# Performance work log

Hardware: AMD Instinct MI355X
Metric: run time of the kernel (lower is better)

## Reference

```python
import jax, jax.numpy as jnp
import numpy as np

B, LQ, LK = 2, 4096, 512
Q_DIM, KV_DIM, D_ATTN, N_HEADS = 1024, 1024, 1024, 16
HDIM = D_ATTN // N_HEADS
LOOKBACK = 4
ROPE_MAX = 8192


def rope_tables(smax, hdim):
    inv_freq = 1.0 / (10000.0 ** (jnp.arange(0, hdim, 2, dtype=jnp.float32) / hdim))
    freqs = jnp.arange(smax, dtype=jnp.float32)[:, None] * inv_freq[None, :]  # [S, hdim/2]
    emb = jnp.concatenate([freqs, freqs], axis=-1)  # [S, hdim]
    return jnp.cos(emb), jnp.sin(emb)


def rotate_half(x):
    h = x.shape[-1] // 2
    return jnp.concatenate([-x[..., h:], x[..., :h]], axis=-1)


def setup_inputs() -> dict:
    key = jax.random.key(0)
    ks = jax.random.split(key, 8)
    q = jax.random.normal(ks[0], (B, LQ, Q_DIM), dtype=jnp.float32)
    kv = jax.random.normal(ks[1], (B, LK, KV_DIM), dtype=jnp.float32)
    q_pos_ids = jax.random.randint(ks[2], (B, LQ), 0, 4096)
    kv_pos_ids = jax.random.randint(ks[3], (LK,), 0, 4096)
    seg_id = jnp.sort(jax.random.randint(ks[4], (B, LQ), 0, LK), axis=-1)
    sc = 1.0 / np.sqrt(Q_DIM)
    Wq = jax.random.normal(ks[5], (Q_DIM, D_ATTN), dtype=jnp.float32) * sc
    Wkv = jax.random.normal(ks[6], (KV_DIM, 2 * D_ATTN), dtype=jnp.float32) * sc
    Wo = jax.random.normal(ks[7], (D_ATTN, Q_DIM), dtype=jnp.float32) * sc
    return {"q": q, "kv": kv, "q_pos_ids": q_pos_ids, "kv_pos_ids": kv_pos_ids,
            "seg_id": seg_id, "Wq": Wq, "Wkv": Wkv, "Wo": Wo}


def reference(q, kv, q_pos_ids, kv_pos_ids, seg_id, Wq, Wkv, Wo):
    Bq, Lq, _ = q.shape
    Lk = kv.shape[1]
    # projections + split heads -> [B, H, L, hdim]
    qh = (q @ Wq).reshape(Bq, Lq, N_HEADS, HDIM).transpose(0, 2, 1, 3)
    kvl = kv @ Wkv
    kh = kvl[..., :D_ATTN].reshape(Bq, Lk, N_HEADS, HDIM).transpose(0, 2, 1, 3)
    vh = kvl[..., D_ATTN:].reshape(Bq, Lk, N_HEADS, HDIM).transpose(0, 2, 1, 3)
    # gathered RoPE
    cos, sin = rope_tables(ROPE_MAX, HDIM)  # [S, hdim]
    qp = jnp.clip(q_pos_ids, 0, ROPE_MAX - 1)
    q_cos = cos[qp][:, None]  # [B,1,Lq,hdim]
    q_sin = sin[qp][:, None]
    qh = qh * q_cos + rotate_half(qh) * q_sin
    kp = jnp.clip(kv_pos_ids, 0, ROPE_MAX - 1)
    k_cos = cos[kp][None, None]  # [1,1,Lk,hdim]
    k_sin = sin[kp][None, None]
    kh = kh * k_cos + rotate_half(kh) * k_sin
    # segment lookback mask: keep iff seg_id - lookback <= k <= seg_id
    kidx = jnp.arange(Lk)
    keep = (kidx[None, None, :] <= seg_id[:, :, None]) & \
           (kidx[None, None, :] >= seg_id[:, :, None] - LOOKBACK)  # [B,Lq,Lk]
    scale = 1.0 / np.sqrt(HDIM)
    scores = jnp.einsum('bhqd,bhkd->bhqk', qh, kh) * scale
    scores = jnp.where(keep[:, None], scores, -jnp.inf)
    attn = jax.nn.softmax(scores, axis=-1)
    ctx = jnp.einsum('bhqk,bhkd->bhqd', attn, vh)
    out = ctx.transpose(0, 2, 1, 3).reshape(Bq, Lq, D_ATTN)
    return out @ Wo
```

## Files before the change

kernel.cpp:

```cpp
#include <hip/hip_runtime.h>
#include <math.h>


typedef unsigned short u16;
typedef __attribute__((ext_vector_type(8))) short bhalf8;
typedef __attribute__((ext_vector_type(4))) float fvec4;

#define MFMA(a, b, c) __builtin_amdgcn_mfma_f32_16x16x32_bf16((a), (b), (c), 0, 0, 0)

__device__ __forceinline__ u16 f2bf(float f) {
  unsigned u = __float_as_uint(f);
  u += 0x7fffu + ((u >> 16) & 1u);
  return (u16)(u >> 16);
}
__device__ __forceinline__ float bf2f(u16 h) {
  return __uint_as_float(((unsigned)h) << 16);
}

__global__ __launch_bounds__(256) void prep_kernel(
    const float* __restrict__ Wq, const float* __restrict__ Wkv,
    const float* __restrict__ Wo, u16* __restrict__ WqT,
    u16* __restrict__ WkvT, u16* __restrict__ WoT,
    const float* __restrict__ q, u16* __restrict__ qb,
    const float* __restrict__ kv, u16* __restrict__ kvb,
    float2* __restrict__ csT) {
  const int bid = blockIdx.x;
  if (bid < 4096) {
    __shared__ float tile[32][33];
    const float* W;
    u16* Wt;
    int N, t;
    if (bid < 1024)      { W = Wq;  Wt = WqT;  N = 1024; t = bid; }
    else if (bid < 3072) { W = Wkv; Wt = WkvT; N = 2048; t = bid - 1024; }
    else                 { W = Wo;  Wt = WoT;  N = 1024; t = bid - 3072; }
    const int sh = (N >> 11) + 5;
    const int n0 = (t & ((1 << sh) - 1)) << 5;
    const int k0 = (t >> sh) << 5;
    const int tx = threadIdx.x & 31, ty = threadIdx.x >> 5;
#pragma unroll
    for (int i = 0; i < 32; i += 8)
      tile[ty + i][tx] = W[(size_t)(k0 + ty + i) * N + n0 + tx];
    __syncthreads();
#pragma unroll
    for (int i = 0; i < 32; i += 8)
      Wt[(size_t)(n0 + ty + i) * 1024 + k0 + tx] = f2bf(tile[tx][ty + i]);
    return;
  }
  const int NQ4 = 2097152, NKV4 = 262144, NR = 131072;
  const int stride = 2048 * 256;
  for (int u = (bid - 4096) * 256 + threadIdx.x; u < NQ4 + NKV4 + NR; u += stride) {
    if (u < NQ4) {
      const float4 v = ((const float4*)q)[u];
      ushort4 o;
      o.x = f2bf(v.x); o.y = f2bf(v.y); o.z = f2bf(v.z); o.w = f2bf(v.w);
      ((ushort4*)qb)[u] = o;
    } else if (u < NQ4 + NKV4) {
      const int i = u - NQ4;
      const float4 v = ((const float4*)kv)[i];
      ushort4 o;
      o.x = f2bf(v.x); o.y = f2bf(v.y); o.z = f2bf(v.z); o.w = f2bf(v.w);
      ((ushort4*)kvb)[i] = o;
    } else {
      const int i = u - NQ4 - NKV4;
      const int pos = i >> 5, j = i & 31;
      const float invf = expf(-(float)j * 0.28782313662425572f);
      float s, c;
      sincosf((float)pos * invf, &s, &c);
      csT[i] = make_float2(c, s);
    }
  }
}

__device__ __forceinline__ void gemm_core_8w(
    const u16* __restrict__ A, const u16* __restrict__ Bt,
    int m0, int n0, fvec4 acc[2][4], u16* As, u16* Bs) {
  const int tid = threadIdx.x;
  const int lane = tid & 63;
  const int wv = tid >> 6, wm = wv >> 1, wn = wv & 1;

  int a_off[2], b_off[4];
#pragma unroll
  for (int i = 0; i < 2; ++i) {
    const int rA = wm * 32 + i * 16 + (lane & 15);
    a_off[i] = rA * 32 + (((lane >> 4) ^ ((rA >> 1) & 3)) << 3);
  }
#pragma unroll
  for (int i = 0; i < 4; ++i) {
    const int rB = wn * 64 + i * 16 + (lane & 15);
    b_off[i] = rB * 32 + (((lane >> 4) ^ ((rB >> 1) & 3)) << 3);
  }
  const int rS = tid >> 2, gS = (tid & 3) ^ ((rS >> 1) & 3);
  const u16* ag = A + (size_t)(m0 + rS) * 1024 + gS * 8;
  const u16* bg = Bt + (size_t)(n0 + rS) * 1024 + gS * 8;
  const int ldst = tid * 8;

#define STAGE2(buf, kk)                                                      \
  do {                                                                       \
    __builtin_amdgcn_global_load_lds(                                        \
        (__attribute__((address_space(1))) void*)(ag + (kk)),                \
        (__attribute__((address_space(3))) void*)(As + (buf) * 4096 + ldst), \
        16, 0, 0);                                                           \
    __builtin_amdgcn_global_load_lds(                                        \
        (__attribute__((address_space(1))) void*)(bg + (kk)),                \
        (__attribute__((address_space(3))) void*)(Bs + (buf) * 4096 + ldst), \
        16, 0, 0);                                                           \
  } while (0)

  STAGE2(0, 0);
  STAGE2(1, 32);
  asm volatile("s_waitcnt vmcnt(2)" ::: "memory");
  __builtin_amdgcn_s_barrier();

#pragma unroll
  for (int t = 0; t < 32; ++t) {
    const int k2 = t * 32 + 64;
    if (k2 < 1024) STAGE2((t + 2) % 3, k2);
    const int co = (t % 3) * 4096;
    bhalf8 af[2], bfv[4];
#pragma unroll
    for (int i = 0; i < 2; ++i) af[i] = *(const bhalf8*)(As + co + a_off[i]);
#pragma unroll
    for (int i = 0; i < 4; ++i) bfv[i] = *(const bhalf8*)(Bs + co + b_off[i]);
    __builtin_amdgcn_s_setprio(1);
#pragma unroll
    for (int mi = 0; mi < 2; ++mi)
#pragma unroll
      for (int ni = 0; ni < 4; ++ni)
        acc[mi][ni] = MFMA(af[mi], bfv[ni], acc[mi][ni]);
    __builtin_amdgcn_s_setprio(0);
    if (k2 < 1024) {
      asm volatile("s_waitcnt vmcnt(2)" ::: "memory");
    } else {
      asm volatile("s_waitcnt vmcnt(0)" ::: "memory");
    }
    __builtin_amdgcn_s_barrier();
  }
#undef STAGE2
}

#define GEMM_PROLOGUE()                                              \
  __shared__ __align__(16) u16 As[3 * 128 * 32];                     \
  __shared__ __align__(16) u16 Bs[3 * 128 * 32];                     \
  fvec4 acc[2][4];                                                   \
  _Pragma("unroll") for (int i = 0; i < 2; ++i)                      \
      _Pragma("unroll") for (int j = 0; j < 4; ++j)                  \
          acc[i][j] = (fvec4){0.f, 0.f, 0.f, 0.f};

__global__ __launch_bounds__(512) void gemm12_kernel(
    const u16* __restrict__ qA, const u16* __restrict__ WqT,
    const u16* __restrict__ kvA, const u16* __restrict__ WkvT,
    u16* __restrict__ qh, u16* __restrict__ kh, u16* __restrict__ vh,
    const int* __restrict__ qpos, const int* __restrict__ kpos,
    const float2* __restrict__ csT) {
  GEMM_PROLOGUE();
  const int swz = ((blockIdx.x & 7) * 80) + (blockIdx.x >> 3);
  const int q5 = swz / 5, r5 = swz - q5 * 5;
  const bool isQ = (r5 < 4);
  const int lane = threadIdx.x & 63;
  const int wv = threadIdx.x >> 6, wm = wv >> 1, wn = wv & 1;

  const u16 *A, *Bt;
  int m0, n0;
  if (isQ) {
    const int id = q5 * 4 + r5;
    A = qA; Bt = WqT;
    m0 = (id >> 3) * 128; n0 = (id & 7) * 128;
  } else {
    const int id = q5;
    A = kvA; Bt = WkvT;
    m0 = (id >> 4) * 128; n0 = (id & 15) * 128;
  }
  gemm_core_8w(A, Bt, m0, n0, acc, As, Bs);

  if (isQ) {
#pragma unroll
    for (int mi = 0; mi < 2; ++mi) {
#pragma unroll
      for (int r = 0; r < 4; ++r) {
        const int rowg = m0 + wm * 32 + mi * 16 + (lane >> 4) * 4 + r;
        int pos = qpos[rowg];
        pos = pos < 0 ? 0 : (pos > 4095 ? 4095 : pos);
#pragma unroll
        for (int ni = 0; ni < 2; ++ni) {
          const int j = ni * 16 + (lane & 15);
          const float2 cs = csT[pos * 32 + j];
          const float x1 = acc[mi][ni][r], x2 = acc[mi][ni + 2][r];
          const int colg = n0 + wn * 64 + ni * 16 + (lane & 15);
          qh[(size_t)rowg * 1024 + colg]      = f2bf((x1 * cs.x - x2 * cs.y) * 0.125f);
          qh[(size_t)rowg * 1024 + colg + 32] = f2bf((x2 * cs.x + x1 * cs.y) * 0.125f);
        }
      }
    }
  } else {
    const bool isK = (n0 + wn * 64) < 1024;
#pragma unroll
    for (int mi = 0; mi < 2; ++mi) {
#pragma unroll
      for (int r = 0; r < 4; ++r) {
        const int rowg = m0 + wm * 32 + mi * 16 + (lane >> 4) * 4 + r;
        if (isK) {
          int pos = kpos[rowg & 511];
          pos = pos < 0 ? 0 : (pos > 4095 ? 4095 : pos);
#pragma unroll
          for (int ni = 0; ni < 2; ++ni) {
            const int j = ni * 16 + (lane & 15);
            const float2 cs = csT[pos * 32 + j];
            const float x1 = acc[mi][ni][r], x2 = acc[mi][ni + 2][r];
            const int colg = n0 + wn * 64 + ni * 16 + (lane & 15);
            kh[(size_t)rowg * 1024 + colg]      = f2bf(x1 * cs.x - x2 * cs.y);
            kh[(size_t)rowg * 1024 + colg + 32] = f2bf(x2 * cs.x + x1 * cs.y);
          }
        } else {
#pragma unroll
          for (int ni = 0; ni < 4; ++ni) {
            const int colg = n0 + wn * 64 + ni * 16 + (lane & 15);
            vh[(size_t)rowg * 1024 + colg - 1024] = f2bf(acc[mi][ni][r]);
          }
        }
      }
    }
  }
}

__global__ __launch_bounds__(512) void gemm_out_kernel(
    const u16* __restrict__ A, const u16* __restrict__ Bt,
    float* __restrict__ out) {
  GEMM_PROLOGUE();
  const int wg = ((blockIdx.x & 7) << 6) + (blockIdx.x >> 3);
  const int m0 = (wg >> 3) * 128, n0 = (wg & 7) * 128;
  gemm_core_8w(A, Bt, m0, n0, acc, As, Bs);
  const int lane = threadIdx.x & 63;
  const int wv = threadIdx.x >> 6, wm = wv >> 1, wn = wv & 1;
#pragma unroll
  for (int mi = 0; mi < 2; ++mi) {
#pragma unroll
    for (int r = 0; r < 4; ++r) {
      const int rowg = m0 + wm * 32 + mi * 16 + (lane >> 4) * 4 + r;
#pragma unroll
      for (int ni = 0; ni < 4; ++ni) {
        const int colg = n0 + wn * 64 + ni * 16 + (lane & 15);
        out[(size_t)rowg * 1024 + colg] = acc[mi][ni][r];
      }
    }
  }
}

__global__ __launch_bounds__(256) void attn_kernel(
    const u16* __restrict__ qh, const u16* __restrict__ kh,
    const u16* __restrict__ vh, const int* __restrict__ seg_id,
    u16* __restrict__ ctx) {
  const int lane = threadIdx.x & 63;
  const int row = (blockIdx.x * 256 + threadIdx.x) >> 6;
  const int b = row >> 12;
  const int sg = seg_id[row];
  const int kmin = sg > 4 ? sg - 4 : 0;

  const u16* qp = qh + (size_t)row * 1024 + lane * 16;
  const bhalf8 qa = *(const bhalf8*)qp;
  const bhalf8 qb = *(const bhalf8*)(qp + 8);
  float qv[16];
#pragma unroll
  for (int e = 0; e < 8; ++e) {
    qv[e] = bf2f((u16)qa[e]);
    qv[8 + e] = bf2f((u16)qb[e]);
  }

  float sc[5];
  float mx = -3.0e38f;
#pragma unroll
  for (int t = 0; t < 5; ++t) {
    const int k = kmin + t;
    const u16* kp = kh + (size_t)((b << 9) + k) * 1024 + lane * 16;
    const bhalf8 ka = *(const bhalf8*)kp;
    const bhalf8 kb = *(const bhalf8*)(kp + 8);
    float d = 0.f;
#pragma unroll
    for (int e = 0; e < 8; ++e)
      d += qv[e] * bf2f((u16)ka[e]) + qv[8 + e] * bf2f((u16)kb[e]);
    d += __shfl_xor(d, 1);
    d += __shfl_xor(d, 2);
    sc[t] = (k <= sg) ? d : -3.0e38f;
    mx = fmaxf(mx, sc[t]);
  }

  float den = 0.f;
  float o[16];
#pragma unroll
  for (int e = 0; e < 16; ++e) o[e] = 0.f;
#pragma unroll
  for (int t = 0; t < 5; ++t) {
    const float p = __expf(sc[t] - mx);
    den += p;
    const int k = kmin + t;
    const u16* vp = vh + (size_t)((b << 9) + k) * 1024 + lane * 16;
    const bhalf8 va = *(const bhalf8*)vp;
    const bhalf8 vb = *(const bhalf8*)(vp + 8);
#pragma unroll
    for (int e = 0; e < 8; ++e) {
      o[e] += p * bf2f((u16)va[e]);
      o[8 + e] += p * bf2f((u16)vb[e]);
    }
  }
  const float inv = 1.f / den;
  bhalf8 oa, ob;
#pragma unroll
  for (int e = 0; e < 8; ++e) {
    oa[e] = (short)f2bf(o[e] * inv);
    ob[e] = (short)f2bf(o[8 + e] * inv);
  }
  u16* cp = ctx + (size_t)row * 1024 + lane * 16;
  *(bhalf8*)cp = oa;
  *(bhalf8*)(cp + 8) = ob;
}

extern "C" void kernel_launch(void* const* d_in, const int* in_sizes, int n_in,
                              void* d_out, int out_size, void* d_ws, size_t ws_size,
                              hipStream_t stream) {
  const float* q   = (const float*)d_in[0];
  const float* kv  = (const float*)d_in[1];
  const int* qpos  = (const int*)d_in[2];
  const int* kpos  = (const int*)d_in[3];
  const int* seg   = (const int*)d_in[4];
  const float* Wq  = (const float*)d_in[5];
  const float* Wkv = (const float*)d_in[6];
  const float* Wo  = (const float*)d_in[7];
  float* out = (float*)d_out;

  char* w = (char*)d_ws;
  u16* qb    = (u16*)w; w += (size_t)8192 * 1024 * 2;
  u16* kvb   = (u16*)w; w += (size_t)1024 * 1024 * 2;
  u16* WqT   = (u16*)w; w += (size_t)1024 * 1024 * 2;
  u16* WkvT  = (u16*)w; w += (size_t)2048 * 1024 * 2;
  u16* WoT   = (u16*)w; w += (size_t)1024 * 1024 * 2;
  u16* qhB   = (u16*)w; w += (size_t)8192 * 1024 * 2;
  u16* khB   = (u16*)w; w += (size_t)1024 * 1024 * 2;
  u16* vhB   = (u16*)w; w += (size_t)1024 * 1024 * 2;
  u16* ctxB  = (u16*)w; w += (size_t)8192 * 1024 * 2;
  float2* csT = (float2*)w; w += (size_t)4096 * 32 * 8;

  prep_kernel<<<6144, 256, 0, stream>>>(Wq, Wkv, Wo, WqT, WkvT, WoT,
                                        q, qb, kv, kvb, csT);
  gemm12_kernel<<<640, 512, 0, stream>>>(qb, WqT, kvb, WkvT,
                                         qhB, khB, vhB, qpos, kpos, csT);
  attn_kernel<<<2048, 256, 0, stream>>>(qhB, khB, vhB, seg, ctxB);
  gemm_out_kernel<<<512, 512, 0, stream>>>(ctxB, WoT, out);
}
```

Measured before the change: 93.10 us.

## Replace 8-wave 128x128 GEMM tiles with single-wave 64x64 barrier-free tiles

Both projection GEMMs move from 512-thread blocks, each computing a 128x128 tile with a triple-buffered LDS pipeline and per-step barriers, to 64-thread single-wave blocks. Each block computes a 64x64 tile with a double-buffered LDS pipeline and needs no s_barrier. The aim is to remove workgroup synchronization, shrink LDS per block and raise block count for better latency hiding. The cost is lower operand reuse per tile, so more global and L2 traffic per FLOP, plus more accumulator registers per wave.

```diff
diff --git a/kernel.cpp b/kernel.cpp
--- a/kernel.cpp
+++ b/kernel.cpp
@@ -71,113 +71,109 @@
   }
 }
 
-__device__ __forceinline__ void gemm_core_8w(
+__device__ __forceinline__ void gemm_core_1w(
     const u16* __restrict__ A, const u16* __restrict__ Bt,
-    int m0, int n0, fvec4 acc[2][4], u16* As, u16* Bs) {
-  const int tid = threadIdx.x;
-  const int lane = tid & 63;
-  const int wv = tid >> 6, wm = wv >> 1, wn = wv & 1;
-
-  int a_off[2], b_off[4];
-#pragma unroll
-  for (int i = 0; i < 2; ++i) {
-    const int rA = wm * 32 + i * 16 + (lane & 15);
-    a_off[i] = rA * 32 + (((lane >> 4) ^ ((rA >> 1) & 3)) << 3);
-  }
+    int m0, int n0, fvec4 acc[4][4], u16* As, u16* Bs) {
+  const int lane = threadIdx.x & 63;
+
+  int off[4];
 #pragma unroll
   for (int i = 0; i < 4; ++i) {
-    const int rB = wn * 64 + i * 16 + (lane & 15);
-    b_off[i] = rB * 32 + (((lane >> 4) ^ ((rB >> 1) & 3)) << 3);
-  }
-  const int rS = tid >> 2, gS = (tid & 3) ^ ((rS >> 1) & 3);
-  const u16* ag = A + (size_t)(m0 + rS) * 1024 + gS * 8;
-  const u16* bg = Bt + (size_t)(n0 + rS) * 1024 + gS * 8;
-  const int ldst = tid * 8;
-
-#define STAGE2(buf, kk)                                                      \
+    const int rr = i * 16 + (lane & 15);
+    off[i] = rr * 32 + (((lane >> 4) ^ ((rr >> 1) & 3)) << 3);
+  }
+  const u16* ag[4];
+  const u16* bg[4];
+#pragma unroll
+  for (int j = 0; j < 4; ++j) {
+    const int c = j * 64 + lane;
+    const int r = c >> 2, g = (c & 3) ^ ((r >> 1) & 3);
+    ag[j] = A + (size_t)(m0 + r) * 1024 + g * 8;
+    bg[j] = Bt + (size_t)(n0 + r) * 1024 + g * 8;
+  }
+  const int l8 = lane * 8;
+
+#define STAGE1W(buf, kk)                                                     \
   do {                                                                       \
-    __builtin_amdgcn_global_load_lds(                                        \
-        (__attribute__((address_space(1))) void*)(ag + (kk)),                \
-        (__attribute__((address_space(3))) void*)(As + (buf) * 4096 + ldst), \
-        16, 0, 0);                                                           \
-    __builtin_amdgcn_global_load_lds(                                        \
-        (__attribute__((address_space(1))) void*)(bg + (kk)),                \
-        (__attribute__((address_space(3))) void*)(Bs + (buf) * 4096 + ldst), \
-        16, 0, 0);                                                           \
+    _Pragma("unroll") for (int j = 0; j < 4; ++j)                            \
+        __builtin_amdgcn_global_load_lds(                                    \
+            (__attribute__((address_space(1))) void*)(ag[j] + (kk)),         \
+            (__attribute__((address_space(3))) void*)(As + (buf) * 2048 +    \
+                                                      j * 512 + l8),         \
+            16, 0, 0);                                                       \
+    _Pragma("unroll") for (int j = 0; j < 4; ++j)                            \
+        __builtin_amdgcn_global_load_lds(                                    \
+            (__attribute__((address_space(1))) void*)(bg[j] + (kk)),         \
+            (__attribute__((address_space(3))) void*)(Bs + (buf) * 2048 +    \
+                                                      j * 512 + l8),         \
+            16, 0, 0);                                                       \
   } while (0)
 
-  STAGE2(0, 0);
-  STAGE2(1, 32);
-  asm volatile("s_waitcnt vmcnt(2)" ::: "memory");
-  __builtin_amdgcn_s_barrier();
-
+  STAGE1W(0, 0);
 #pragma unroll
   for (int t = 0; t < 32; ++t) {
-    const int k2 = t * 32 + 64;
-    if (k2 < 1024) STAGE2((t + 2) % 3, k2);
-    const int co = (t % 3) * 4096;
-    bhalf8 af[2], bfv[4];
-#pragma unroll
-    for (int i = 0; i < 2; ++i) af[i] = *(const bhalf8*)(As + co + a_off[i]);
-#pragma unroll
-    for (int i = 0; i < 4; ++i) bfv[i] = *(const bhalf8*)(Bs + co + b_off[i]);
+    if (t < 31) {
+      STAGE1W((t + 1) & 1, (t + 1) * 32);
+      asm volatile("s_waitcnt vmcnt(8)" ::: "memory");
+    } else {
+      asm volatile("s_waitcnt vmcnt(0)" ::: "memory");
+    }
+    const int co = (t & 1) * 2048;
+    bhalf8 af[4], bfv[4];
+#pragma unroll
+    for (int i = 0; i < 4; ++i) af[i] = *(const bhalf8*)(As + co + off[i]);
+#pragma unroll
+    for (int i = 0; i < 4; ++i) bfv[i] = *(const bhalf8*)(Bs + co + off[i]);
     __builtin_amdgcn_s_setprio(1);
 #pragma unroll
-    for (int mi = 0; mi < 2; ++mi)
+    for (int mi = 0; mi < 4; ++mi)
 #pragma unroll
       for (int ni = 0; ni < 4; ++ni)
         acc[mi][ni] = MFMA(af[mi], bfv[ni], acc[mi][ni]);
     __builtin_amdgcn_s_setprio(0);
-    if (k2 < 1024) {
-      asm volatile("s_waitcnt vmcnt(2)" ::: "memory");
-    } else {
-      asm volatile("s_waitcnt vmcnt(0)" ::: "memory");
-    }
-    __builtin_amdgcn_s_barrier();
-  }
-#undef STAGE2
+  }
+#undef STAGE1W
 }
 
 #define GEMM_PROLOGUE()                                              \
-  __shared__ __align__(16) u16 As[3 * 128 * 32];                     \
-  __shared__ __align__(16) u16 Bs[3 * 128 * 32];                     \
-  fvec4 acc[2][4];                                                   \
-  _Pragma("unroll") for (int i = 0; i < 2; ++i)                      \
+  __shared__ __align__(16) u16 As[2 * 2048];                         \
+  __shared__ __align__(16) u16 Bs[2 * 2048];                         \
+  fvec4 acc[4][4];                                                   \
+  _Pragma("unroll") for (int i = 0; i < 4; ++i)                      \
       _Pragma("unroll") for (int j = 0; j < 4; ++j)                  \
           acc[i][j] = (fvec4){0.f, 0.f, 0.f, 0.f};
 
-__global__ __launch_bounds__(512) void gemm12_kernel(
+__global__ __launch_bounds__(64) void gemm12_kernel(
     const u16* __restrict__ qA, const u16* __restrict__ WqT,
     const u16* __restrict__ kvA, const u16* __restrict__ WkvT,
     u16* __restrict__ qh, u16* __restrict__ kh, u16* __restrict__ vh,
     const int* __restrict__ qpos, const int* __restrict__ kpos,
     const float2* __restrict__ csT) {
   GEMM_PROLOGUE();
-  const int swz = ((blockIdx.x & 7) * 80) + (blockIdx.x >> 3);
+  const int swz = ((blockIdx.x & 7) * 320) + (blockIdx.x >> 3);
   const int q5 = swz / 5, r5 = swz - q5 * 5;
   const bool isQ = (r5 < 4);
   const int lane = threadIdx.x & 63;
-  const int wv = threadIdx.x >> 6, wm = wv >> 1, wn = wv & 1;
-
-  const u16 *A, *Bt;
+
+  const u16 *Aop, *Bop;
   int m0, n0;
   if (isQ) {
     const int id = q5 * 4 + r5;
-    A = qA; Bt = WqT;
-    m0 = (id >> 3) * 128; n0 = (id & 7) * 128;
+    Aop = qA; Bop = WqT;
+    m0 = (id >> 4) * 64; n0 = (id & 15) * 64;
   } else {
     const int id = q5;
-    A = kvA; Bt = WkvT;
-    m0 = (id >> 4) * 128; n0 = (id & 15) * 128;
-  }
-  gemm_core_8w(A, Bt, m0, n0, acc, As, Bs);
+    Aop = kvA; Bop = WkvT;
+    m0 = (id >> 5) * 64; n0 = (id & 31) * 64;
+  }
+  gemm_core_1w(Aop, Bop, m0, n0, acc, As, Bs);
 
   if (isQ) {
 #pragma unroll
-    for (int mi = 0; mi < 2; ++mi) {
+    for (int mi = 0; mi < 4; ++mi) {
 #pragma unroll
       for (int r = 0; r < 4; ++r) {
-        const int rowg = m0 + wm * 32 + mi * 16 + (lane >> 4) * 4 + r;
+        const int rowg = m0 + mi * 16 + (lane >> 4) * 4 + r;
         int pos = qpos[rowg];
         pos = pos < 0 ? 0 : (pos > 4095 ? 4095 : pos);
 #pragma unroll
@@ -185,19 +181,19 @@
           const int j = ni * 16 + (lane & 15);
           const float2 cs = csT[pos * 32 + j];
           const float x1 = acc[mi][ni][r], x2 = acc[mi][ni + 2][r];
-          const int colg = n0 + wn * 64 + ni * 16 + (lane & 15);
+          const int colg = n0 + ni * 16 + (lane & 15);
           qh[(size_t)rowg * 1024 + colg]      = f2bf((x1 * cs.x - x2 * cs.y) * 0.125f);
           qh[(size_t)rowg * 1024 + colg + 32] = f2bf((x2 * cs.x + x1 * cs.y) * 0.125f);
         }
       }
     }
   } else {
-    const bool isK = (n0 + wn * 64) < 1024;
-#pragma unroll
-    for (int mi = 0; mi < 2; ++mi) {
+    const bool isK = n0 < 1024;
+#pragma unroll
+    for (int mi = 0; mi < 4; ++mi) {
 #pragma unroll
       for (int r = 0; r < 4; ++r) {
-        const int rowg = m0 + wm * 32 + mi * 16 + (lane >> 4) * 4 + r;
+        const int rowg = m0 + mi * 16 + (lane >> 4) * 4 + r;
         if (isK) {
           int pos = kpos[rowg & 511];
           pos = pos < 0 ? 0 : (pos > 4095 ? 4095 : pos);
@@ -206,14 +202,14 @@
             const int j = ni * 16 + (lane & 15);
             const float2 cs = csT[pos * 32 + j];
             const float x1 = acc[mi][ni][r], x2 = acc[mi][ni + 2][r];
-            const int colg = n0 + wn * 64 + ni * 16 + (lane & 15);
+            const int colg = n0 + ni * 16 + (lane & 15);
             kh[(size_t)rowg * 1024 + colg]      = f2bf(x1 * cs.x - x2 * cs.y);
             kh[(size_t)rowg * 1024 + colg + 32] = f2bf(x2 * cs.x + x1 * cs.y);
           }
         } else {
 #pragma unroll
           for (int ni = 0; ni < 4; ++ni) {
-            const int colg = n0 + wn * 64 + ni * 16 + (lane & 15);
+            const int colg = n0 + ni * 16 + (lane & 15);
             vh[(size_t)rowg * 1024 + colg - 1024] = f2bf(acc[mi][ni][r]);
           }
         }
@@ -222,23 +218,22 @@
   }
 }
 
-__global__ __launch_bounds__(512) void gemm_out_kernel(
+__global__ __launch_bounds__(64) void gemm_out_kernel(
     const u16* __restrict__ A, const u16* __restrict__ Bt,
     float* __restrict__ out) {
   GEMM_PROLOGUE();
-  const int wg = ((blockIdx.x & 7) << 6) + (blockIdx.x >> 3);
-  const int m0 = (wg >> 3) * 128, n0 = (wg & 7) * 128;
-  gemm_core_8w(A, Bt, m0, n0, acc, As, Bs);
+  const int swz = ((blockIdx.x & 7) << 8) + (blockIdx.x >> 3);
+  const int m0 = (swz >> 4) * 64, n0 = (swz & 15) * 64;
+  gemm_core_1w(A, Bt, m0, n0, acc, As, Bs);
   const int lane = threadIdx.x & 63;
-  const int wv = threadIdx.x >> 6, wm = wv >> 1, wn = wv & 1;
-#pragma unroll
-  for (int mi = 0; mi < 2; ++mi) {
+#pragma unroll
+  for (int mi = 0; mi < 4; ++mi) {
 #pragma unroll
     for (int r = 0; r < 4; ++r) {
-      const int rowg = m0 + wm * 32 + mi * 16 + (lane >> 4) * 4 + r;
+      const int rowg = m0 + mi * 16 + (lane >> 4) * 4 + r;
 #pragma unroll
       for (int ni = 0; ni < 4; ++ni) {
-        const int colg = n0 + wn * 64 + ni * 16 + (lane & 15);
+        const int colg = n0 + ni * 16 + (lane & 15);
         out[(size_t)rowg * 1024 + colg] = acc[mi][ni][r];
       }
     }
@@ -340,8 +335,8 @@
 
   prep_kernel<<<6144, 256, 0, stream>>>(Wq, Wkv, Wo, WqT, WkvT, WoT,
                                         q, qb, kv, kvb, csT);
-  gemm12_kernel<<<640, 512, 0, stream>>>(qb, WqT, kvb, WkvT,
+  gemm12_kernel<<<2560, 64, 0, stream>>>(qb, WqT, kvb, WkvT,
                                          qhB, khB, vhB, qpos, kpos, csT);
   attn_kernel<<<2048, 256, 0, stream>>>(qhB, khB, vhB, seg, ctxB);
-  gemm_out_kernel<<<512, 512, 0, stream>>>(ctxB, WoT, out);
-}
+  gemm_out_kernel<<<2048, 64, 0, stream>>>(ctxB, WoT, out);
+}
```

Measured after the change: 116.1 us. 1.25x slower.
